# Performance work log

Measured on AMD Instinct MI355X. Metric: run time of the kernel, lower is better.

The kernel has to match this reference:

```python
import jax, jax.numpy as jnp
import numpy as np

B, T, H = 8192, 24, 1024


def setup_inputs() -> dict:
    key = jax.random.key(0)
    ks = jax.random.split(key, 16)
    n = lambda k, shp, s=1.0: (jax.random.normal(k, shp, dtype=jnp.float32) * s)
    return {
        "x": n(ks[0], (B, T, 1)),
        "h1_0": n(ks[1], (B, H), 0.02),
        "c1_0": n(ks[2], (B, H), 0.02),
        "h2_0": n(ks[3], (B, H), 0.02),
        "c2_0": n(ks[4], (B, H), 0.02),
        "W_ih1": n(ks[5], (4 * H, 1), 0.05),
        "W_hh1": n(ks[6], (4 * H, H), 0.02),
        "b_ih1": n(ks[7], (4 * H,), 0.02),
        "b_hh1": n(ks[8], (4 * H,), 0.02),
        "W_ih2": n(ks[9], (4 * H, H), 0.02),
        "W_hh2": n(ks[10], (4 * H, H), 0.02),
        "b_ih2": n(ks[11], (4 * H,), 0.02),
        "b_hh2": n(ks[12], (4 * H,), 0.02),
        "W_out": n(ks[13], (2, H), 0.02),
        "b_out": jnp.array([0.2, -0.2], dtype=jnp.float32),
    }


def _lstm_cell(x_t, h, c, W_ih, W_hh, b_ih, b_hh):
    # PyTorch LSTMCell: gates ordered (i, f, g, o)
    gates = x_t @ W_ih.T + b_ih + h @ W_hh.T + b_hh  # [B, 4H]
    i, f, g, o = jnp.split(gates, 4, axis=-1)
    c_new = jax.nn.sigmoid(f) * c + jax.nn.sigmoid(i) * jnp.tanh(g)
    h_new = jax.nn.sigmoid(o) * jnp.tanh(c_new)
    return h_new, c_new


def reference(x, h1_0, c1_0, h2_0, c2_0,
              W_ih1, W_hh1, b_ih1, b_hh1,
              W_ih2, W_hh2, b_ih2, b_hh2,
              W_out, b_out):
    xs = jnp.transpose(x, (1, 0, 2))  # [T, B, 1]

    def step(carry, x_t):
        h1, c1, h2, c2 = carry
        h1, c1 = _lstm_cell(x_t, h1, c1, W_ih1, W_hh1, b_ih1, b_hh1)
        h2, c2 = _lstm_cell(h1, h2, c2, W_ih2, W_hh2, b_ih2, b_hh2)
        return (h1, c1, h2, c2), None

    (h1, c1, h2, c2), _ = jax.lax.scan(step, (h1_0, c1_0, h2_0, c2_0), xs)
    return h2 @ W_out.T + b_out  # [B, 2]
```

## Files before the change

kernel.cpp:

```cpp
#include <hip/hip_runtime.h>
#include <hip/hip_bf16.h>
#include <stdint.h>

#define B_SZ 8192
#define T_SZ 24
#define H_SZ 1024
#define G4   4096

typedef __attribute__((ext_vector_type(8))) short bf16x8;
typedef __attribute__((ext_vector_type(4))) float f32x4;

__device__ __forceinline__ int perm_old(int p) {
    int gate = (p >> 4) & 3;
    int unit = ((p >> 6) << 4) | (p & 15);
    return gate * 1024 + unit;
}

__device__ __forceinline__ float fast_sigmoid(float x) {
    return 1.f / (1.f + __expf(-x));
}
__device__ __forceinline__ float fast_tanh(float x) {
    float ax = __builtin_fabsf(x);
    float e  = __expf(2.f * ax);
    float r  = 1.f - 2.f / (e + 1.f);
    return __builtin_copysignf(r, x);
}

__global__ void k_prep_w1(const float* __restrict__ Whh1, __hip_bfloat16* __restrict__ dst) {
    int i = blockIdx.x * blockDim.x + threadIdx.x;
    int p = i >> 10, k = i & 1023;
    dst[i] = __float2bfloat16(Whh1[(size_t)perm_old(p) * 1024 + k]);
}

__global__ void k_prep_w2(const float* __restrict__ Wih2, const float* __restrict__ Whh2,
                          __hip_bfloat16* __restrict__ dst) {
    int i = blockIdx.x * blockDim.x + threadIdx.x;
    int p = i >> 11, k = i & 2047;
    int old = perm_old(p);
    float v = (k < 1024) ? Wih2[(size_t)old * 1024 + k] : Whh2[(size_t)old * 1024 + (k - 1024)];
    dst[i] = __float2bfloat16(v);
}

__global__ void k_prep_vec(const float* __restrict__ bih1, const float* __restrict__ bhh1,
                           const float* __restrict__ bih2, const float* __restrict__ bhh2,
                           const float* __restrict__ Wih1,
                           float* __restrict__ b1p, float* __restrict__ b2p,
                           float* __restrict__ w1p) {
    int p = blockIdx.x * blockDim.x + threadIdx.x;
    if (p >= G4) return;
    int old = perm_old(p);
    b1p[p] = bih1[old] + bhh1[old];
    b2p[p] = bih2[old] + bhh2[old];
    w1p[p] = Wih1[old];
}

__global__ void k_xT(const float* __restrict__ x, float* __restrict__ xT) {
    int i = blockIdx.x * blockDim.x + threadIdx.x;
    if (i >= B_SZ * T_SZ) return;
    int b = i / T_SZ, t = i % T_SZ;
    xT[t * B_SZ + b] = x[i];
}

__global__ void k_init_state(const float* __restrict__ h1_0, const float* __restrict__ c1_0,
                             const float* __restrict__ h2_0, const float* __restrict__ c2_0,
                             __hip_bfloat16* __restrict__ A2_0, __hip_bfloat16* __restrict__ A2_1,
                             float* __restrict__ c1, float* __restrict__ c2) {
    int i = blockIdx.x * blockDim.x + threadIdx.x;
    if (i >= B_SZ * H_SZ) return;
    int b = i >> 10, j = i & 1023;
    A2_1[(size_t)b * 2048 + j]        = __float2bfloat16(h1_0[i]);
    A2_0[(size_t)b * 2048 + 1024 + j] = __float2bfloat16(h2_0[i]);
    c1[i] = c1_0[i];
    c2[i] = c2_0[i];
}

#define BM 256
#define BN 256
#define BK 64

template<int LAYER>
__global__ __launch_bounds__(512, 2)
void k_gemm_cell(const __hip_bfloat16* __restrict__ A, int lda,
                 const __hip_bfloat16* __restrict__ Bw, int ldb, int K,
                 const float* __restrict__ biasp, const float* __restrict__ wih1p,
                 const float* __restrict__ xT, int t,
                 float* __restrict__ c, __hip_bfloat16* __restrict__ hout) {
    __shared__ short As[2][BM][BK];
    __shared__ short Bs[2][BN][BK];
    const int tid  = threadIdx.x;
    const int lane = tid & 63;
    const int wid  = tid >> 6;

    const int bid = blockIdx.x;
    const int xcd = bid & 7;
    const int i   = bid >> 3;
    const int ml  = (i & 7) | ((i >> 5) << 3);
    const int nl  = (i >> 3) & 3;
    const int m0  = ((xcd & 1) * 16 + ml) * BM;
    const int n0  = ((xcd >> 1) * 4 + nl) * BN;

    const int wm = wid >> 2;
    const int wn = wid & 3;
    const int fr = lane & 15;
    const int kg = lane >> 4;

    const __hip_bfloat16* Abase = A  + (size_t)m0 * lda;
    const __hip_bfloat16* Bbase = Bw + (size_t)n0 * ldb;

    f32x4 acc[8][4];
#pragma unroll
    for (int ii = 0; ii < 8; ++ii)
#pragma unroll
        for (int j = 0; j < 4; ++j) acc[ii][j] = (f32x4)0.f;

    auto stage8A = [&](int buf, int lr0, int kcol) {
        int lr = lr0 + (lane >> 3);
        int scol = (((lane & 7) ^ (lr & 7)) << 3);
        const __hip_bfloat16* gp = Abase + (size_t)lr * lda + kcol + scol;
        __builtin_amdgcn_global_load_lds(
            (const __attribute__((address_space(1))) void*)gp,
            (__attribute__((address_space(3))) void*)(&As[buf][lr0][0]), 16, 0, 0);
    };
    auto stage8B = [&](int buf, int lr0, int kcol) {
        int lr = lr0 + (lane >> 3);
        int scol = (((lane & 7) ^ (lr & 7)) << 3);
        const __hip_bfloat16* gp = Bbase + (size_t)lr * ldb + kcol + scol;
        __builtin_amdgcn_global_load_lds(
            (const __attribute__((address_space(1))) void*)gp,
            (__attribute__((address_space(3))) void*)(&Bs[buf][lr0][0]), 16, 0, 0);
    };
    auto stage_u1 = [&](int kt, int buf) {
#pragma unroll
        for (int j = 0; j < 2; ++j) {
            int rr0 = (wid * 2 + j) * 8;
            int lr0 = (rr0 < 64) ? rr0 : rr0 + 64;
            stage8A(buf, lr0, kt * BK);
        }
    };
    auto stage_u2 = [&](int kt, int buf) {
#pragma unroll
        for (int j = 0; j < 2; ++j) {
            int rr0 = (wid * 2 + j) * 8;
            int lr0 = (rr0 < 64) ? rr0 + 64 : rr0 + 128;
            stage8A(buf, lr0, kt * BK);
        }
    };
    auto stage_u3 = [&](int kt, int buf) {
#pragma unroll
        for (int j = 0; j < 2; ++j) {
            int rr0 = (wid * 2 + j) * 8;
            int lr0 = ((rr0 >> 5) << 6) + (rr0 & 31);
            stage8B(buf, lr0, kt * BK);
        }
    };
    auto stage_u4 = [&](int kt, int buf) {
#pragma unroll
        for (int j = 0; j < 2; ++j) {
            int rr0 = (wid * 2 + j) * 8;
            int lr0 = ((rr0 >> 5) << 6) + 32 + (rr0 & 31);
            stage8B(buf, lr0, kt * BK);
        }
    };

    const int aoff = (wm * 128 + fr) * 64;
    const int boff = (wn * 64 + fr) * 64;
    const int ck8_0 = ((kg ^ (fr & 7)) << 3);
    const int ck8_1 = (((4 + kg) ^ (fr & 7)) << 3);
    const short* As0 = &As[0][0][0];
    const short* As1 = &As[1][0][0];
    const short* Bs0 = &Bs[0][0][0];
    const short* Bs1 = &Bs[1][0][0];

    const int NK = K >> 6;

    stage_u1(0, 0); stage_u3(0, 0); stage_u2(0, 0); stage_u4(0, 0);
    stage_u1(1, 1); stage_u3(1, 1); stage_u4(1, 1); stage_u2(1, 1);
    asm volatile("s_waitcnt vmcnt(8)" ::: "memory");
    __builtin_amdgcn_s_barrier();

    bf16x8 a0[4][2], a1[4][2], b0[2][2], b1[2][2];

    for (int kt = 0; kt < NK; ++kt) {
        const int buf = kt & 1;
        const short* as = buf ? As1 : As0;
        const short* bs = buf ? Bs1 : Bs0;

#pragma unroll
        for (int m = 0; m < 4; ++m) {
            a0[m][0] = *(const bf16x8*)(as + aoff + m * 1024 + ck8_0);
            a0[m][1] = *(const bf16x8*)(as + aoff + m * 1024 + ck8_1);
        }
#pragma unroll
        for (int n = 0; n < 2; ++n) {
            b0[n][0] = *(const bf16x8*)(bs + boff + n * 1024 + ck8_0);
            b0[n][1] = *(const bf16x8*)(bs + boff + n * 1024 + ck8_1);
        }
        asm volatile("s_waitcnt lgkmcnt(8)" ::: "memory");
        __builtin_amdgcn_s_barrier();
        asm volatile("s_waitcnt lgkmcnt(0)" ::: "memory");
        __builtin_amdgcn_s_setprio(1);
#pragma unroll
        for (int ks = 0; ks < 2; ++ks)
#pragma unroll
            for (int m = 0; m < 4; ++m)
#pragma unroll
                for (int n = 0; n < 2; ++n)
                    acc[m][n] = __builtin_amdgcn_mfma_f32_16x16x32_bf16(a0[m][ks], b0[n][ks], acc[m][n], 0, 0, 0);
        __builtin_amdgcn_s_setprio(0);
        __builtin_amdgcn_s_barrier();

#pragma unroll
        for (int n = 0; n < 2; ++n) {
            b1[n][0] = *(const bf16x8*)(bs + boff + (2 + n) * 1024 + ck8_0);
            b1[n][1] = *(const bf16x8*)(bs + boff + (2 + n) * 1024 + ck8_1);
        }
        if (kt + 2 < NK) { stage_u1(kt + 2, buf); stage_u3(kt + 2, buf); }
        __builtin_amdgcn_s_barrier();
        asm volatile("s_waitcnt lgkmcnt(0)" ::: "memory");
        __builtin_amdgcn_s_setprio(1);
#pragma unroll
        for (int ks = 0; ks < 2; ++ks)
#pragma unroll
            for (int m = 0; m < 4; ++m)
#pragma unroll
                for (int n = 0; n < 2; ++n)
                    acc[m][2 + n] = __builtin_amdgcn_mfma_f32_16x16x32_bf16(a0[m][ks], b1[n][ks], acc[m][2 + n], 0, 0, 0);
        __builtin_amdgcn_s_setprio(0);
        __builtin_amdgcn_s_barrier();

#pragma unroll
        for (int m = 0; m < 4; ++m) {
            a1[m][0] = *(const bf16x8*)(as + aoff + (4 + m) * 1024 + ck8_0);
            a1[m][1] = *(const bf16x8*)(as + aoff + (4 + m) * 1024 + ck8_1);
        }
        if (kt + 2 < NK) stage_u4(kt + 2, buf);
        __builtin_amdgcn_s_barrier();
        asm volatile("s_waitcnt lgkmcnt(0)" ::: "memory");
        __builtin_amdgcn_s_setprio(1);
#pragma unroll
        for (int ks = 0; ks < 2; ++ks)
#pragma unroll
            for (int m = 0; m < 4; ++m)
#pragma unroll
                for (int n = 0; n < 2; ++n)
                    acc[4 + m][n] = __builtin_amdgcn_mfma_f32_16x16x32_bf16(a1[m][ks], b0[n][ks], acc[4 + m][n], 0, 0, 0);
        __builtin_amdgcn_s_setprio(0);
        __builtin_amdgcn_s_barrier();

        if (kt + 2 < NK) stage_u2(kt + 2, buf);
        __builtin_amdgcn_s_barrier();
        __builtin_amdgcn_s_setprio(1);
#pragma unroll
        for (int ks = 0; ks < 2; ++ks)
#pragma unroll
            for (int m = 0; m < 4; ++m)
#pragma unroll
                for (int n = 0; n < 2; ++n)
                    acc[4 + m][2 + n] = __builtin_amdgcn_mfma_f32_16x16x32_bf16(a1[m][ks], b1[n][ks], acc[4 + m][2 + n], 0, 0, 0);
        __builtin_amdgcn_s_setprio(0);
        if (kt + 2 < NK)      asm volatile("s_waitcnt vmcnt(8)" ::: "memory");
        else if (kt + 1 < NK) asm volatile("s_waitcnt vmcnt(0)" ::: "memory");
        __builtin_amdgcn_s_barrier();
    }

    float biasv[4], xwv[4];
#pragma unroll
    for (int n = 0; n < 4; ++n) {
        int col = n0 + wn * 64 + n * 16 + fr;
        biasv[n] = biasp[col];
        if (LAYER == 1) xwv[n] = wih1p[col];
    }
    const int u = ((n0 >> 6) + wn) * 16 + fr;

#pragma unroll
    for (int m = 0; m < 8; ++m) {
        int rbase = m0 + wm * 128 + m * 16 + (lane >> 4) * 4;
#pragma unroll
        for (int j = 0; j < 4; ++j) {
            int b = rbase + j;
            float gi = acc[m][0][j] + biasv[0];
            float gf = acc[m][1][j] + biasv[1];
            float gg = acc[m][2][j] + biasv[2];
            float go = acc[m][3][j] + biasv[3];
            if (LAYER == 1) {
                float xv = xT[t * B_SZ + b];
                gi += xv * xwv[0];
                gf += xv * xwv[1];
                gg += xv * xwv[2];
                go += xv * xwv[3];
            }
            float si = fast_sigmoid(gi);
            float sf = fast_sigmoid(gf);
            float so = fast_sigmoid(go);
            float tg = fast_tanh(gg);
            size_t ci = (size_t)b * H_SZ + u;
            float cn = sf * c[ci] + si * tg;
            c[ci] = cn;
            hout[(size_t)b * 2048 + u] = __float2bfloat16(so * fast_tanh(cn));
        }
    }
}

__global__ __launch_bounds__(256)
void k_out(const __hip_bfloat16* __restrict__ h2base, const float* __restrict__ Wout,
           const float* __restrict__ bout, float* __restrict__ out) {
    int gw   = (blockIdx.x * blockDim.x + threadIdx.x) >> 6;
    int lane = threadIdx.x & 63;
    if (gw >= B_SZ) return;
    const __hip_bfloat16* h = h2base + (size_t)gw * 2048;
    float a0 = 0.f, a1 = 0.f;
#pragma unroll
    for (int k = lane; k < 1024; k += 64) {
        float hv = __bfloat162float(h[k]);
        a0 += hv * Wout[k];
        a1 += hv * Wout[1024 + k];
    }
    for (int off = 32; off; off >>= 1) {
        a0 += __shfl_down(a0, off);
        a1 += __shfl_down(a1, off);
    }
    if (lane == 0) {
        out[gw * 2 + 0] = a0 + bout[0];
        out[gw * 2 + 1] = a1 + bout[1];
    }
}

extern "C" void kernel_launch(void* const* d_in, const int* in_sizes, int n_in,
                              void* d_out, int out_size, void* d_ws, size_t ws_size,
                              hipStream_t stream) {
    const float* x    = (const float*)d_in[0];
    const float* h1_0 = (const float*)d_in[1];
    const float* c1_0 = (const float*)d_in[2];
    const float* h2_0 = (const float*)d_in[3];
    const float* c2_0 = (const float*)d_in[4];
    const float* Wih1 = (const float*)d_in[5];
    const float* Whh1 = (const float*)d_in[6];
    const float* bih1 = (const float*)d_in[7];
    const float* bhh1 = (const float*)d_in[8];
    const float* Wih2 = (const float*)d_in[9];
    const float* Whh2 = (const float*)d_in[10];
    const float* bih2 = (const float*)d_in[11];
    const float* bhh2 = (const float*)d_in[12];
    const float* Wout = (const float*)d_in[13];
    const float* bout = (const float*)d_in[14];
    float* out = (float*)d_out;
    (void)in_sizes; (void)n_in; (void)out_size; (void)ws_size;

    uint8_t* ws = (uint8_t*)d_ws;
    size_t off = 0;
    auto alloc = [&](size_t bytes) { void* p = ws + off; off += (bytes + 255) & ~(size_t)255; return p; };
    __hip_bfloat16* A2_0  = (__hip_bfloat16*)alloc((size_t)B_SZ * 2048 * 2);
    __hip_bfloat16* A2_1  = (__hip_bfloat16*)alloc((size_t)B_SZ * 2048 * 2);
    float*          c1    = (float*)alloc((size_t)B_SZ * H_SZ * 4);
    float*          c2    = (float*)alloc((size_t)B_SZ * H_SZ * 4);
    __hip_bfloat16* Whh1p = (__hip_bfloat16*)alloc((size_t)G4 * H_SZ * 2);
    __hip_bfloat16* Wcat2p= (__hip_bfloat16*)alloc((size_t)G4 * 2048 * 2);
    float*          bias1p= (float*)alloc(G4 * 4);
    float*          bias2p= (float*)alloc(G4 * 4);
    float*          wih1p = (float*)alloc(G4 * 4);
    float*          xT    = (float*)alloc((size_t)T_SZ * B_SZ * 4);

    __hip_bfloat16* A2[2] = { A2_0, A2_1 };

    k_prep_w1<<<(G4 * H_SZ + 255) / 256, 256, 0, stream>>>(Whh1, Whh1p);
    k_prep_w2<<<(G4 * 2048 + 255) / 256, 256, 0, stream>>>(Wih2, Whh2, Wcat2p);
    k_prep_vec<<<(G4 + 255) / 256, 256, 0, stream>>>(bih1, bhh1, bih2, bhh2, Wih1,
                                                     bias1p, bias2p, wih1p);
    k_xT<<<(B_SZ * T_SZ + 255) / 256, 256, 0, stream>>>(x, xT);
    k_init_state<<<(B_SZ * H_SZ + 255) / 256, 256, 0, stream>>>(h1_0, c1_0, h2_0, c2_0,
                                                                A2_0, A2_1, c1, c2);

    const int gemm_blocks = (B_SZ / BM) * (G4 / BN);

    for (int t = 0; t < T_SZ; ++t) {
        __hip_bfloat16* Pprev = A2[(t + 1) & 1];
        __hip_bfloat16* Pt    = A2[t & 1];
        k_gemm_cell<1><<<gemm_blocks, 512, 0, stream>>>(
            (const __hip_bfloat16*)Pprev, 2048, Whh1p, 1024, 1024,
            bias1p, wih1p, xT, t, c1, Pt);
        k_gemm_cell<2><<<gemm_blocks, 512, 0, stream>>>(
            (const __hip_bfloat16*)Pt, 2048, Wcat2p, 2048, 2048,
            bias2p, nullptr, nullptr, 0, c2, A2[(t + 1) & 1] + 1024);
    }
    k_out<<<(B_SZ * 64 + 255) / 256, 256, 0, stream>>>(A2_0 + 1024, Wout, bout, out);
}
```

Baseline: 5.496 ms.

## Switch LSTM GEMM to 32x32 MFMA with two N-tiles per block

Replaces the 16x16x32 MFMA tiles with 32x32x16 bf16 MFMA, so the gate-row permutation and LDS swizzle change to match the new accumulator layout. Gate values are paired across lanes with shuffles in the epilogue. Each block now loops over two consecutive N tiles, which halves the grid to about one block per pair and gives it a simpler M-major mapping in place of the XCD-aware one. The bias and input-weight permutation is dropped, and raw vectors are indexed directly. The aim is fewer LDS reads per FLOP and better MFMA throughput, at the cost of extra shuffles, predicated epilogue lanes and less parallelism per launch.

```diff
diff --git a/kernel.cpp b/kernel.cpp
--- a/kernel.cpp
+++ b/kernel.cpp
@@ -8,13 +8,14 @@
 #define G4   4096
 
 typedef __attribute__((ext_vector_type(8))) short bf16x8;
-typedef __attribute__((ext_vector_type(4))) float f32x4;
+typedef __attribute__((ext_vector_type(16))) float f32x16;
 
 __device__ __forceinline__ int perm_old(int p) {
-    int gate = (p >> 4) & 3;
+    int gate = ((p >> 5) & 1) * 2 + ((p >> 4) & 1);
     int unit = ((p >> 6) << 4) | (p & 15);
     return gate * 1024 + unit;
 }
+__device__ __forceinline__ int swz8(int r) { return (r ^ (r >> 3)) & 7; }
 
 __device__ __forceinline__ float fast_sigmoid(float x) {
     return 1.f / (1.f + __expf(-x));
@@ -43,15 +44,11 @@
 
 __global__ void k_prep_vec(const float* __restrict__ bih1, const float* __restrict__ bhh1,
                            const float* __restrict__ bih2, const float* __restrict__ bhh2,
-                           const float* __restrict__ Wih1,
-                           float* __restrict__ b1p, float* __restrict__ b2p,
-                           float* __restrict__ w1p) {
+                           float* __restrict__ b1p, float* __restrict__ b2p) {
     int p = blockIdx.x * blockDim.x + threadIdx.x;
     if (p >= G4) return;
-    int old = perm_old(p);
-    b1p[p] = bih1[old] + bhh1[old];
-    b2p[p] = bih2[old] + bhh2[old];
-    w1p[p] = Wih1[old];
+    b1p[p] = bih1[p] + bhh1[p];
+    b2p[p] = bih2[p] + bhh2[p];
 }
 
 __global__ void k_xT(const float* __restrict__ x, float* __restrict__ xT) {
@@ -82,222 +79,209 @@
 __global__ __launch_bounds__(512, 2)
 void k_gemm_cell(const __hip_bfloat16* __restrict__ A, int lda,
                  const __hip_bfloat16* __restrict__ Bw, int ldb, int K,
-                 const float* __restrict__ biasp, const float* __restrict__ wih1p,
+                 const float* __restrict__ biasp, const float* __restrict__ wih1,
                  const float* __restrict__ xT, int t,
                  float* __restrict__ c, __hip_bfloat16* __restrict__ hout) {
     __shared__ short As[2][BM][BK];
     __shared__ short Bs[2][BN][BK];
-    const int tid  = threadIdx.x;
-    const int lane = tid & 63;
-    const int wid  = tid >> 6;
-
-    const int bid = blockIdx.x;
-    const int xcd = bid & 7;
-    const int i   = bid >> 3;
-    const int ml  = (i & 7) | ((i >> 5) << 3);
-    const int nl  = (i >> 3) & 3;
-    const int m0  = ((xcd & 1) * 16 + ml) * BM;
-    const int n0  = ((xcd >> 1) * 4 + nl) * BN;
-
-    const int wm = wid >> 2;
-    const int wn = wid & 3;
-    const int fr = lane & 15;
-    const int kg = lane >> 4;
-
-    const __hip_bfloat16* Abase = A  + (size_t)m0 * lda;
-    const __hip_bfloat16* Bbase = Bw + (size_t)n0 * ldb;
-
-    f32x4 acc[8][4];
-#pragma unroll
-    for (int ii = 0; ii < 8; ++ii)
-#pragma unroll
-        for (int j = 0; j < 4; ++j) acc[ii][j] = (f32x4)0.f;
-
-    auto stage8A = [&](int buf, int lr0, int kcol) {
-        int lr = lr0 + (lane >> 3);
-        int scol = (((lane & 7) ^ (lr & 7)) << 3);
-        const __hip_bfloat16* gp = Abase + (size_t)lr * lda + kcol + scol;
-        __builtin_amdgcn_global_load_lds(
-            (const __attribute__((address_space(1))) void*)gp,
-            (__attribute__((address_space(3))) void*)(&As[buf][lr0][0]), 16, 0, 0);
-    };
-    auto stage8B = [&](int buf, int lr0, int kcol) {
-        int lr = lr0 + (lane >> 3);
-        int scol = (((lane & 7) ^ (lr & 7)) << 3);
-        const __hip_bfloat16* gp = Bbase + (size_t)lr * ldb + kcol + scol;
-        __builtin_amdgcn_global_load_lds(
-            (const __attribute__((address_space(1))) void*)gp,
-            (__attribute__((address_space(3))) void*)(&Bs[buf][lr0][0]), 16, 0, 0);
-    };
-    auto stage_u1 = [&](int kt, int buf) {
-#pragma unroll
-        for (int j = 0; j < 2; ++j) {
-            int rr0 = (wid * 2 + j) * 8;
-            int lr0 = (rr0 < 64) ? rr0 : rr0 + 64;
-            stage8A(buf, lr0, kt * BK);
+    const int lane = threadIdx.x & 63;
+    const int wid  = threadIdx.x >> 6;
+
+    const int bid   = blockIdx.x;
+    const int npair = bid & 7;
+    const int m0    = (bid >> 3) * BM;
+
+    const int wm  = wid >> 2;
+    const int wn  = wid & 3;
+    const int l31 = lane & 31;
+    const int kg  = lane >> 5;
+
+    const __hip_bfloat16* Abase = A + (size_t)m0 * lda;
+    const int NK = K >> 6;
+
+    for (int half = 0; half < 2; ++half) {
+        const int n0 = (npair * 2 + half) * BN;
+        const __hip_bfloat16* Bbase = Bw + (size_t)n0 * ldb;
+
+        f32x16 acc[4][2];
+#pragma unroll
+        for (int ii = 0; ii < 4; ++ii)
+#pragma unroll
+            for (int jj = 0; jj < 2; ++jj) acc[ii][jj] = (f32x16)0.f;
+
+        auto stage8A = [&](int buf, int lr0, int kcol) {
+            int lr = lr0 + (lane >> 3);
+            int scol = (((lane & 7) ^ swz8(lr)) << 3);
+            const __hip_bfloat16* gp = Abase + (size_t)lr * lda + kcol + scol;
+            __builtin_amdgcn_global_load_lds(
+                (const __attribute__((address_space(1))) void*)gp,
+                (__attribute__((address_space(3))) void*)(&As[buf][lr0][0]), 16, 0, 0);
+        };
+        auto stage8B = [&](int buf, int lr0, int kcol) {
+            int lr = lr0 + (lane >> 3);
+            int scol = (((lane & 7) ^ swz8(lr)) << 3);
+            const __hip_bfloat16* gp = Bbase + (size_t)lr * ldb + kcol + scol;
+            __builtin_amdgcn_global_load_lds(
+                (const __attribute__((address_space(1))) void*)gp,
+                (__attribute__((address_space(3))) void*)(&Bs[buf][lr0][0]), 16, 0, 0);
+        };
+        auto stage_u1 = [&](int kt, int buf) {
+#pragma unroll
+            for (int j = 0; j < 2; ++j) {
+                int rr0 = (wid * 2 + j) * 8;
+                int lr0 = (rr0 < 64) ? rr0 : rr0 + 64;
+                stage8A(buf, lr0, kt * BK);
+            }
+        };
+        auto stage_u2 = [&](int kt, int buf) {
+#pragma unroll
+            for (int j = 0; j < 2; ++j) {
+                int rr0 = (wid * 2 + j) * 8;
+                int lr0 = (rr0 < 64) ? rr0 + 64 : rr0 + 128;
+                stage8A(buf, lr0, kt * BK);
+            }
+        };
+        auto stage_u3 = [&](int kt, int buf) {
+#pragma unroll
+            for (int j = 0; j < 2; ++j) {
+                int rr0 = (wid * 2 + j) * 8;
+                int lr0 = ((rr0 >> 5) << 6) + (rr0 & 31);
+                stage8B(buf, lr0, kt * BK);
+            }
+        };
+        auto stage_u4 = [&](int kt, int buf) {
+#pragma unroll
+            for (int j = 0; j < 2; ++j) {
+                int rr0 = (wid * 2 + j) * 8;
+                int lr0 = ((rr0 >> 5) << 6) + 32 + (rr0 & 31);
+                stage8B(buf, lr0, kt * BK);
+            }
+        };
+
+        auto rdA = [&](const short* as, int mt, int ks) -> bf16x8 {
+            int row = wm * 128 + mt * 32 + l31;
+            int ch = (ks * 2 + kg) ^ swz8(row);
+            return *(const bf16x8*)(as + row * 64 + ch * 8);
+        };
+        auto rdB = [&](const short* bs, int nt, int ks) -> bf16x8 {
+            int row = wn * 64 + nt * 32 + l31;
+            int ch = (ks * 2 + kg) ^ swz8(row);
+            return *(const bf16x8*)(bs + row * 64 + ch * 8);
+        };
+
+        stage_u1(0, 0); stage_u3(0, 0); stage_u2(0, 0); stage_u4(0, 0);
+        stage_u1(1, 1); stage_u3(1, 1); stage_u4(1, 1); stage_u2(1, 1);
+        asm volatile("s_waitcnt vmcnt(8)" ::: "memory");
+        __builtin_amdgcn_s_barrier();
+
+        bf16x8 a0[2][4], a1[2][4], b0[4], b1[4];
+
+        for (int kt = 0; kt < NK; ++kt) {
+            const int buf = kt & 1;
+            const short* as = buf ? &As[1][0][0] : &As[0][0][0];
+            const short* bs = buf ? &Bs[1][0][0] : &Bs[0][0][0];
+
+#pragma unroll
+            for (int mt = 0; mt < 2; ++mt)
+#pragma unroll
+                for (int ks = 0; ks < 4; ++ks) a0[mt][ks] = rdA(as, mt, ks);
+#pragma unroll
+            for (int ks = 0; ks < 4; ++ks) b0[ks] = rdB(bs, 0, ks);
+            asm volatile("s_waitcnt lgkmcnt(8)" ::: "memory");
+            __builtin_amdgcn_s_barrier();
+            asm volatile("s_waitcnt lgkmcnt(0)" ::: "memory");
+            __builtin_amdgcn_s_setprio(1);
+#pragma unroll
+            for (int ks = 0; ks < 4; ++ks)
+#pragma unroll
+                for (int mt = 0; mt < 2; ++mt)
+                    acc[mt][0] = __builtin_amdgcn_mfma_f32_32x32x16_bf16(a0[mt][ks], b0[ks], acc[mt][0], 0, 0, 0);
+            __builtin_amdgcn_s_setprio(0);
+            __builtin_amdgcn_s_barrier();
+
+#pragma unroll
+            for (int ks = 0; ks < 4; ++ks) b1[ks] = rdB(bs, 1, ks);
+            if (kt + 2 < NK) { stage_u1(kt + 2, buf); stage_u3(kt + 2, buf); }
+            __builtin_amdgcn_s_barrier();
+            asm volatile("s_waitcnt lgkmcnt(0)" ::: "memory");
+            __builtin_amdgcn_s_setprio(1);
+#pragma unroll
+            for (int ks = 0; ks < 4; ++ks)
+#pragma unroll
+                for (int mt = 0; mt < 2; ++mt)
+                    acc[mt][1] = __builtin_amdgcn_mfma_f32_32x32x16_bf16(a0[mt][ks], b1[ks], acc[mt][1], 0, 0, 0);
+            __builtin_amdgcn_s_setprio(0);
+            __builtin_amdgcn_s_barrier();
+
+#pragma unroll
+            for (int mt = 0; mt < 2; ++mt)
+#pragma unroll
+                for (int ks = 0; ks < 4; ++ks) a1[mt][ks] = rdA(as, 2 + mt, ks);
+            if (kt + 2 < NK) stage_u4(kt + 2, buf);
+            __builtin_amdgcn_s_barrier();
+            asm volatile("s_waitcnt lgkmcnt(0)" ::: "memory");
+            __builtin_amdgcn_s_setprio(1);
+#pragma unroll
+            for (int ks = 0; ks < 4; ++ks)
+#pragma unroll
+                for (int mt = 0; mt < 2; ++mt)
+                    acc[2 + mt][0] = __builtin_amdgcn_mfma_f32_32x32x16_bf16(a1[mt][ks], b0[ks], acc[2 + mt][0], 0, 0, 0);
+            __builtin_amdgcn_s_setprio(0);
+            __builtin_amdgcn_s_barrier();
+
+            if (kt + 2 < NK) stage_u2(kt + 2, buf);
+            __builtin_amdgcn_s_barrier();
+            __builtin_amdgcn_s_setprio(1);
+#pragma unroll
+            for (int ks = 0; ks < 4; ++ks)
+#pragma unroll
+                for (int mt = 0; mt < 2; ++mt)
+                    acc[2 + mt][1] = __builtin_amdgcn_mfma_f32_32x32x16_bf16(a1[mt][ks], b1[ks], acc[2 + mt][1], 0, 0, 0);
+            __builtin_amdgcn_s_setprio(0);
+            if (kt + 2 < NK)      asm volatile("s_waitcnt vmcnt(8)" ::: "memory");
+            else if (kt + 1 < NK) asm volatile("s_waitcnt vmcnt(0)" ::: "memory");
+            __builtin_amdgcn_s_barrier();
         }
-    };
-    auto stage_u2 = [&](int kt, int buf) {
-#pragma unroll
-        for (int j = 0; j < 2; ++j) {
-            int rr0 = (wid * 2 + j) * 8;
-            int lr0 = (rr0 < 64) ? rr0 + 64 : rr0 + 128;
-            stage8A(buf, lr0, kt * BK);
+
+        const int U0 = ((n0 + wn * 64) >> 6) * 16;
+        const int u  = U0 + (lane & 15);
+        float bgi = biasp[u],        bgf = biasp[1024 + u];
+        float bgg = biasp[2048 + u], bgo = biasp[3072 + u];
+        float xwi = 0.f, xwf = 0.f, xwg = 0.f, xwo = 0.f;
+        if (LAYER == 1) {
+            xwi = wih1[u]; xwf = wih1[1024 + u]; xwg = wih1[2048 + u]; xwo = wih1[3072 + u];
         }
-    };
-    auto stage_u3 = [&](int kt, int buf) {
-#pragma unroll
-        for (int j = 0; j < 2; ++j) {
-            int rr0 = (wid * 2 + j) * 8;
-            int lr0 = ((rr0 >> 5) << 6) + (rr0 & 31);
-            stage8B(buf, lr0, kt * BK);
+        const int myhalf = (lane >> 4) & 1;
+        const int rext   = (lane >> 5) * 4;
+
+#pragma unroll
+        for (int mt = 0; mt < 4; ++mt) {
+#pragma unroll
+            for (int r = 0; r < 16; ++r) {
+                float t0 = __shfl_xor(acc[mt][0][r], 16);
+                float t1 = __shfl_xor(acc[mt][1][r], 16);
+                if ((r >> 3) == myhalf) {
+                    float gi = (myhalf ? t0 : acc[mt][0][r]) + bgi;
+                    float gf = (myhalf ? acc[mt][0][r] : t0) + bgf;
+                    float gg = (myhalf ? t1 : acc[mt][1][r]) + bgg;
+                    float go = (myhalf ? acc[mt][1][r] : t1) + bgo;
+                    int b = m0 + wm * 128 + mt * 32 + (r & 3) + 8 * (r >> 2) + rext;
+                    if (LAYER == 1) {
+                        float xv = xT[t * B_SZ + b];
+                        gi += xv * xwi; gf += xv * xwf; gg += xv * xwg; go += xv * xwo;
+                    }
+                    float si = fast_sigmoid(gi);
+                    float sf = fast_sigmoid(gf);
+                    float so = fast_sigmoid(go);
+                    float tg = fast_tanh(gg);
+                    size_t ci = (size_t)b * H_SZ + u;
+                    float cn = sf * c[ci] + si * tg;
+                    c[ci] = cn;
+                    hout[(size_t)b * 2048 + u] = __float2bfloat16(so * fast_tanh(cn));
+                }
+            }
         }
-    };
-    auto stage_u4 = [&](int kt, int buf) {
-#pragma unroll
-        for (int j = 0; j < 2; ++j) {
-            int rr0 = (wid * 2 + j) * 8;
-            int lr0 = ((rr0 >> 5) << 6) + 32 + (rr0 & 31);
-            stage8B(buf, lr0, kt * BK);
-        }
-    };
-
-    const int aoff = (wm * 128 + fr) * 64;
-    const int boff = (wn * 64 + fr) * 64;
-    const int ck8_0 = ((kg ^ (fr & 7)) << 3);
-    const int ck8_1 = (((4 + kg) ^ (fr & 7)) << 3);
-    const short* As0 = &As[0][0][0];
-    const short* As1 = &As[1][0][0];
-    const short* Bs0 = &Bs[0][0][0];
-    const short* Bs1 = &Bs[1][0][0];
-
-    const int NK = K >> 6;
-
-    stage_u1(0, 0); stage_u3(0, 0); stage_u2(0, 0); stage_u4(0, 0);
-    stage_u1(1, 1); stage_u3(1, 1); stage_u4(1, 1); stage_u2(1, 1);
-    asm volatile("s_waitcnt vmcnt(8)" ::: "memory");
-    __builtin_amdgcn_s_barrier();
-
-    bf16x8 a0[4][2], a1[4][2], b0[2][2], b1[2][2];
-
-    for (int kt = 0; kt < NK; ++kt) {
-        const int buf = kt & 1;
-        const short* as = buf ? As1 : As0;
-        const short* bs = buf ? Bs1 : Bs0;
-
-#pragma unroll
-        for (int m = 0; m < 4; ++m) {
-            a0[m][0] = *(const bf16x8*)(as + aoff + m * 1024 + ck8_0);
-            a0[m][1] = *(const bf16x8*)(as + aoff + m * 1024 + ck8_1);
-        }
-#pragma unroll
-        for (int n = 0; n < 2; ++n) {
-            b0[n][0] = *(const bf16x8*)(bs + boff + n * 1024 + ck8_0);
-            b0[n][1] = *(const bf16x8*)(bs + boff + n * 1024 + ck8_1);
-        }
-        asm volatile("s_waitcnt lgkmcnt(8)" ::: "memory");
         __builtin_amdgcn_s_barrier();
-        asm volatile("s_waitcnt lgkmcnt(0)" ::: "memory");
-        __builtin_amdgcn_s_setprio(1);
-#pragma unroll
-        for (int ks = 0; ks < 2; ++ks)
-#pragma unroll
-            for (int m = 0; m < 4; ++m)
-#pragma unroll
-                for (int n = 0; n < 2; ++n)
-                    acc[m][n] = __builtin_amdgcn_mfma_f32_16x16x32_bf16(a0[m][ks], b0[n][ks], acc[m][n], 0, 0, 0);
-        __builtin_amdgcn_s_setprio(0);
-        __builtin_amdgcn_s_barrier();
-
-#pragma unroll
-        for (int n = 0; n < 2; ++n) {
-            b1[n][0] = *(const bf16x8*)(bs + boff + (2 + n) * 1024 + ck8_0);
-            b1[n][1] = *(const bf16x8*)(bs + boff + (2 + n) * 1024 + ck8_1);
-        }
-        if (kt + 2 < NK) { stage_u1(kt + 2, buf); stage_u3(kt + 2, buf); }
-        __builtin_amdgcn_s_barrier();
-        asm volatile("s_waitcnt lgkmcnt(0)" ::: "memory");
-        __builtin_amdgcn_s_setprio(1);
-#pragma unroll
-        for (int ks = 0; ks < 2; ++ks)
-#pragma unroll
-            for (int m = 0; m < 4; ++m)
-#pragma unroll
-                for (int n = 0; n < 2; ++n)
-                    acc[m][2 + n] = __builtin_amdgcn_mfma_f32_16x16x32_bf16(a0[m][ks], b1[n][ks], acc[m][2 + n], 0, 0, 0);
-        __builtin_amdgcn_s_setprio(0);
-        __builtin_amdgcn_s_barrier();
-
-#pragma unroll
-        for (int m = 0; m < 4; ++m) {
-            a1[m][0] = *(const bf16x8*)(as + aoff + (4 + m) * 1024 + ck8_0);
-            a1[m][1] = *(const bf16x8*)(as + aoff + (4 + m) * 1024 + ck8_1);
-        }
-        if (kt + 2 < NK) stage_u4(kt + 2, buf);
-        __builtin_amdgcn_s_barrier();
-        asm volatile("s_waitcnt lgkmcnt(0)" ::: "memory");
-        __builtin_amdgcn_s_setprio(1);
-#pragma unroll
-        for (int ks = 0; ks < 2; ++ks)
-#pragma unroll
-            for (int m = 0; m < 4; ++m)
-#pragma unroll
-                for (int n = 0; n < 2; ++n)
-                    acc[4 + m][n] = __builtin_amdgcn_mfma_f32_16x16x32_bf16(a1[m][ks], b0[n][ks], acc[4 + m][n], 0, 0, 0);
-        __builtin_amdgcn_s_setprio(0);
-        __builtin_amdgcn_s_barrier();
-
-        if (kt + 2 < NK) stage_u2(kt + 2, buf);
-        __builtin_amdgcn_s_barrier();
-        __builtin_amdgcn_s_setprio(1);
-#pragma unroll
-        for (int ks = 0; ks < 2; ++ks)
-#pragma unroll
-            for (int m = 0; m < 4; ++m)
-#pragma unroll
-                for (int n = 0; n < 2; ++n)
-                    acc[4 + m][2 + n] = __builtin_amdgcn_mfma_f32_16x16x32_bf16(a1[m][ks], b1[n][ks], acc[4 + m][2 + n], 0, 0, 0);
-        __builtin_amdgcn_s_setprio(0);
-        if (kt + 2 < NK)      asm volatile("s_waitcnt vmcnt(8)" ::: "memory");
-        else if (kt + 1 < NK) asm volatile("s_waitcnt vmcnt(0)" ::: "memory");
-        __builtin_amdgcn_s_barrier();
-    }
-
-    float biasv[4], xwv[4];
-#pragma unroll
-    for (int n = 0; n < 4; ++n) {
-        int col = n0 + wn * 64 + n * 16 + fr;
-        biasv[n] = biasp[col];
-        if (LAYER == 1) xwv[n] = wih1p[col];
-    }
-    const int u = ((n0 >> 6) + wn) * 16 + fr;
-
-#pragma unroll
-    for (int m = 0; m < 8; ++m) {
-        int rbase = m0 + wm * 128 + m * 16 + (lane >> 4) * 4;
-#pragma unroll
-        for (int j = 0; j < 4; ++j) {
-            int b = rbase + j;
-            float gi = acc[m][0][j] + biasv[0];
-            float gf = acc[m][1][j] + biasv[1];
-            float gg = acc[m][2][j] + biasv[2];
-            float go = acc[m][3][j] + biasv[3];
-            if (LAYER == 1) {
-                float xv = xT[t * B_SZ + b];
-                gi += xv * xwv[0];
-                gf += xv * xwv[1];
-                gg += xv * xwv[2];
-                go += xv * xwv[3];
-            }
-            float si = fast_sigmoid(gi);
-            float sf = fast_sigmoid(gf);
-            float so = fast_sigmoid(go);
-            float tg = fast_tanh(gg);
-            size_t ci = (size_t)b * H_SZ + u;
-            float cn = sf * c[ci] + si * tg;
-            c[ci] = cn;
-            hout[(size_t)b * 2048 + u] = __float2bfloat16(so * fast_tanh(cn));
-        }
     }
 }
 
@@ -357,27 +341,25 @@
     __hip_bfloat16* Wcat2p= (__hip_bfloat16*)alloc((size_t)G4 * 2048 * 2);
     float*          bias1p= (float*)alloc(G4 * 4);
     float*          bias2p= (float*)alloc(G4 * 4);
-    float*          wih1p = (float*)alloc(G4 * 4);
     float*          xT    = (float*)alloc((size_t)T_SZ * B_SZ * 4);
 
     __hip_bfloat16* A2[2] = { A2_0, A2_1 };
 
     k_prep_w1<<<(G4 * H_SZ + 255) / 256, 256, 0, stream>>>(Whh1, Whh1p);
     k_prep_w2<<<(G4 * 2048 + 255) / 256, 256, 0, stream>>>(Wih2, Whh2, Wcat2p);
-    k_prep_vec<<<(G4 + 255) / 256, 256, 0, stream>>>(bih1, bhh1, bih2, bhh2, Wih1,
-                                                     bias1p, bias2p, wih1p);
+    k_prep_vec<<<(G4 + 255) / 256, 256, 0, stream>>>(bih1, bhh1, bih2, bhh2, bias1p, bias2p);
     k_xT<<<(B_SZ * T_SZ + 255) / 256, 256, 0, stream>>>(x, xT);
     k_init_state<<<(B_SZ * H_SZ + 255) / 256, 256, 0, stream>>>(h1_0, c1_0, h2_0, c2_0,
                                                                 A2_0, A2_1, c1, c2);
 
-    const int gemm_blocks = (B_SZ / BM) * (G4 / BN);
+    const int gemm_blocks = (B_SZ / BM) * (G4 / BN) / 2;
 
     for (int t = 0; t < T_SZ; ++t) {
         __hip_bfloat16* Pprev = A2[(t + 1) & 1];
         __hip_bfloat16* Pt    = A2[t & 1];
         k_gemm_cell<1><<<gemm_blocks, 512, 0, stream>>>(
             (const __hip_bfloat16*)Pprev, 2048, Whh1p, 1024, 1024,
-            bias1p, wih1p, xT, t, c1, Pt);
+            bias1p, Wih1, xT, t, c1, Pt);
         k_gemm_cell<2><<<gemm_blocks, 512, 0, stream>>>(
             (const __hip_bfloat16*)Pt, 2048, Wcat2p, 2048, 2048,
             bias2p, nullptr, nullptr, 0, c2, A2[(t + 1) & 1] + 1024);
```

Result: slower. 11.81 ms (+114.9%).
